# Optimization experiments

Measured on AMD Instinct MI355X. Metric: run time of the kernel, lower is better.

The kernel has to match this reference:

```python
import jax, jax.numpy as jnp
import numpy as np

B, S, DM, H, DK, DH = 8, 1024, 512, 8, 32, 64
LN_EPS = 1e-5
NEG_SLOPE = 0.01  # torch LeakyReLU default


def _l2norm(t, axis=-1, eps=1e-12):
    # matches F.normalize(p=2): x / max(||x||, eps)
    n = jnp.sqrt(jnp.sum(t * t, axis=axis, keepdims=True))
    return t / jnp.maximum(n, eps)


def _layernorm(t, w, b, eps=LN_EPS):
    mu = jnp.mean(t, axis=-1, keepdims=True)
    var = jnp.mean((t - mu) ** 2, axis=-1, keepdims=True)
    return (t - mu) * jax.lax.rsqrt(var + eps) * w + b


def setup_inputs() -> dict:
    key = jax.random.key(0)
    ks = jax.random.split(key, 16)
    x = jax.random.normal(ks[0], (B, S, DM), dtype=jnp.float32)
    # causal-style mask: True = masked (upper triangle)
    attn_mask = jnp.broadcast_to(jnp.triu(jnp.ones((S, S), dtype=bool), k=1), (B, S, S))
    pairwise_dist = jax.random.uniform(ks[1], (B, S, S), dtype=jnp.float32)
    s = 0.02
    return {
        "x": x,
        "attn_mask": attn_mask,
        "pairwise_dist": pairwise_dist,
        "Wq": jax.random.normal(ks[2], (H, DK, DM), dtype=jnp.float32) * s,
        "Wk": jax.random.normal(ks[3], (H, DK, DM), dtype=jnp.float32) * s,
        "Wv": jax.random.normal(ks[4], (H, DH, DM), dtype=jnp.float32) * s,
        "omega": jnp.ones((H,), dtype=jnp.float32),
        "Wo": jax.random.normal(ks[5], (DM, H * DH), dtype=jnp.float32) * s,
        "bo": jnp.zeros((DM,), dtype=jnp.float32),
        "Wf": jax.random.normal(ks[6], (DM, DM), dtype=jnp.float32) * s,
        "bf": jnp.zeros((DM,), dtype=jnp.float32),
        "ln1_w": jnp.ones((DM,), dtype=jnp.float32),
        "ln1_b": jnp.zeros((DM,), dtype=jnp.float32),
        "ln2_w": jnp.ones((DM,), dtype=jnp.float32),
        "ln2_b": jnp.zeros((DM,), dtype=jnp.float32),
    }


def _encoder_layer(x, attn_mask, pairwise_dist, Wq, Wk, Wv, omega,
                   Wo, bo, Wf, bf, ln1_w, ln1_b, ln2_w, ln2_b):
    # --- multi-head self-attention, all heads batched ---
    q = _l2norm(jnp.einsum('bsd,hkd->hbsk', x, Wq))   # [H,B,S,DK]
    k = _l2norm(jnp.einsum('bsd,hkd->hbsk', x, Wk))
    v = jnp.einsum('bsd,hvd->hbsv', x, Wv)            # [H,B,S,DH]
    scores = jnp.einsum('hbsk,hbtk->hbst', q, k)      # cosine-sim, [H,B,S,S]
    # distance bias: exp(-omega*d) - 1, detached in the original
    r = jax.lax.stop_gradient(
        jnp.exp(-omega[:, None, None, None] * pairwise_dist[None]) - 1.0)
    scores = scores + r
    scores = jnp.where(attn_mask[None], -jnp.inf, scores)
    # custom softmax: exp(x) / (sum + 1); exp(-inf)=0 handles masking
    z = jnp.exp(scores)
    attn = z / (jnp.sum(z, axis=-1, keepdims=True) + 1.0)
    y = jnp.einsum('hbst,hbtv->hbsv', attn, v)        # [H,B,S,DH]
    y = jnp.transpose(y, (1, 2, 0, 3)).reshape(x.shape[0], x.shape[1], -1)  # concat heads
    x_attn = y @ Wo.T + bo
    # --- residual + LN + FFN (dropout p=0 -> identity) ---
    z1 = _layernorm(x + x_attn, ln1_w, ln1_b)
    z_ff = jax.nn.leaky_relu(z1 @ Wf.T + bf, negative_slope=NEG_SLOPE)
    return _layernorm(z1 + z_ff, ln2_w, ln2_b)


def reference(x, attn_mask, pairwise_dist, Wq, Wk, Wv, omega,
              Wo, bo, Wf, bf, ln1_w, ln1_b, ln2_w, ln2_b):
    return _encoder_layer(x, attn_mask, pairwise_dist, Wq, Wk, Wv, omega,
                          Wo, bo, Wf, bf, ln1_w, ln1_b, ln2_w, ln2_b)
```

## Files before the change

kernel.cpp:

```cpp
#include <hip/hip_runtime.h>
#include <hip/hip_bf16.h>
#include <math.h>
#include <stdint.h>

#define BB 8
#define SS 1024
#define DMM 512
#define HH 8
#define DKK 32
#define DHH 64

typedef __bf16 bf16x8 __attribute__((ext_vector_type(8)));
typedef float f32x4 __attribute__((ext_vector_type(4)));

__device__ __forceinline__ void gll16(const void* g, void* l) {
  __builtin_amdgcn_global_load_lds(
      (const __attribute__((address_space(1))) void*)(uintptr_t)g,
      (__attribute__((address_space(3))) void*)(uint32_t)(uintptr_t)l,
      16, 0, 0);
}

__device__ __forceinline__ uint4 pack8(const float4 a, const float4 b) {
  union { __hip_bfloat162 h2[4]; uint4 u; } p;
  p.h2[0] = __float22bfloat162_rn(make_float2(a.x, a.y));
  p.h2[1] = __float22bfloat162_rn(make_float2(a.z, a.w));
  p.h2[2] = __float22bfloat162_rn(make_float2(b.x, b.y));
  p.h2[3] = __float22bfloat162_rn(make_float2(b.z, b.w));
  return p.u;
}

__global__ __launch_bounds__(256) void cvt_pre(
    const float* __restrict__ x, const float* __restrict__ Wq,
    const float* __restrict__ Wk, const float* __restrict__ Wv,
    __bf16* __restrict__ xb, __bf16* __restrict__ Wcat) {
  size_t i = ((size_t)blockIdx.x * 256 + threadIdx.x) * 8;
  const float* s;
  __bf16* d;
  size_t off;
  if (i < 4194304) { s = x; d = xb; off = i; }
  else {
    size_t j = i - 4194304;
    d = Wcat + j;
    if (j < 131072) { s = Wq; off = j; }
    else if (j < 262144) { s = Wk; off = j - 131072; }
    else { s = Wv; off = j - 262144; }
    d = Wcat + j - off + off;
    float4 a = *(const float4*)&s[off];
    float4 b = *(const float4*)&s[off + 4];
    *(uint4*)&Wcat[j] = pack8(a, b);
    return;
  }
  float4 a = *(const float4*)&s[off];
  float4 b = *(const float4*)&s[off + 4];
  *(uint4*)&d[off] = pack8(a, b);
}

__global__ __launch_bounds__(256) void cvt_wof(
    const float* __restrict__ Wo, const float* __restrict__ Wf,
    __bf16* __restrict__ dWo, __bf16* __restrict__ dWf) {
  size_t i = ((size_t)blockIdx.x * 256 + threadIdx.x) * 8;
  const float* s;
  __bf16* d;
  size_t off;
  if (i < 262144) { s = Wo; d = dWo; off = i; }
  else { s = Wf; d = dWf; off = i - 262144; }
  float4 a = *(const float4*)&s[off];
  float4 b = *(const float4*)&s[off + 4];
  *(uint4*)&d[off] = pack8(a, b);
}

template <int MODE>
__global__ __launch_bounds__(256) void gemm_bf16(
    const __bf16* __restrict__ A, const __bf16* __restrict__ W,
    const float* __restrict__ bias, const float* __restrict__ resid,
    float* __restrict__ C, int N) {
  __shared__ __bf16 As[128 * 32];
  __shared__ __bf16 Bs[128 * 32];
  const int tid = threadIdx.x;
  const int n0 = blockIdx.x * 128;
  const int m0 = blockIdx.y * 128;
  const int lane = tid & 63;
  const int w = tid >> 6;
  const int wm = (w & 1) * 64, wn = (w >> 1) * 64;
  const int fr = lane & 15, quad = lane >> 4;

  const int srow = lane >> 2;
  const int schunk = (lane & 3) ^ ((lane >> 3) & 3);

  f32x4 acc[4][4];
#pragma unroll
  for (int mi = 0; mi < 4; ++mi)
#pragma unroll
    for (int ni = 0; ni < 4; ++ni) acc[mi][ni] = (f32x4){0.f, 0.f, 0.f, 0.f};

  for (int kt = 0; kt < 512; kt += 32) {
    __syncthreads();
#pragma unroll
    for (int j = 0; j < 2; ++j) {
      const int seg = w * 2 + j;
      const int row = seg * 16 + srow;
      gll16(&A[(size_t)(m0 + row) * 512 + kt + schunk * 8], &As[seg * 512]);
      gll16(&W[(size_t)(n0 + row) * 512 + kt + schunk * 8], &Bs[seg * 512]);
    }
    __syncthreads();

    bf16x8 af[4], bf[4];
    const int rsw = (quad ^ ((fr >> 1) & 3)) * 8;
#pragma unroll
    for (int mi = 0; mi < 4; ++mi)
      af[mi] = *(const bf16x8*)&As[(wm + mi * 16 + fr) * 32 + rsw];
#pragma unroll
    for (int ni = 0; ni < 4; ++ni)
      bf[ni] = *(const bf16x8*)&Bs[(wn + ni * 16 + fr) * 32 + rsw];
#pragma unroll
    for (int mi = 0; mi < 4; ++mi)
#pragma unroll
      for (int ni = 0; ni < 4; ++ni)
        acc[mi][ni] = __builtin_amdgcn_mfma_f32_16x16x32_bf16(
            af[mi], bf[ni], acc[mi][ni], 0, 0, 0);
  }

  const int er = (lane >> 4) * 4;
  const int ec = lane & 15;
#pragma unroll
  for (int mi = 0; mi < 4; ++mi) {
#pragma unroll
    for (int ni = 0; ni < 4; ++ni) {
      const int n = n0 + wn + ni * 16 + ec;
      float bsv = (MODE != 0) ? bias[n] : 0.0f;
#pragma unroll
      for (int r = 0; r < 4; ++r) {
        const int m = m0 + wm + mi * 16 + er + r;
        float v = acc[mi][ni][r];
        if (MODE == 1) {
          v += bsv + resid[(size_t)m * 512 + n];
        } else if (MODE == 2) {
          float g = v + bsv;
          g = g > 0.f ? g : 0.01f * g;
          v = resid[(size_t)m * 512 + n] + g;
        }
        C[(size_t)m * N + n] = v;
      }
    }
  }
}

__global__ __launch_bounds__(256) void prep_qkv(
    const float* __restrict__ qkv, __bf16* __restrict__ Qg,
    __bf16* __restrict__ Kg, __bf16* __restrict__ Vt) {
  __shared__ __bf16 vt[64][136];
  const int bh = blockIdx.x;
  const int b = bh >> 3, h = bh & 7;
  const int sb = blockIdx.y * 128;
  const int tid = threadIdx.x;

  {
    const int row = tid >> 1, half = tid & 1;
    const size_t rb = ((size_t)b * 1024 + sb + row) * 1024;
    {
      const float* p = qkv + rb + h * 32 + half * 16;
      float4 a[4];
      float ss = 0.f;
#pragma unroll
      for (int i = 0; i < 4; ++i) {
        a[i] = ((const float4*)p)[i];
        ss += a[i].x * a[i].x + a[i].y * a[i].y + a[i].z * a[i].z + a[i].w * a[i].w;
      }
      ss += __shfl_xor(ss, 1, 64);
      float sc = 1.0f / fmaxf(sqrtf(ss), 1e-12f);
      float4 s0 = make_float4(a[0].x * sc, a[0].y * sc, a[0].z * sc, a[0].w * sc);
      float4 s1 = make_float4(a[1].x * sc, a[1].y * sc, a[1].z * sc, a[1].w * sc);
      float4 s2 = make_float4(a[2].x * sc, a[2].y * sc, a[2].z * sc, a[2].w * sc);
      float4 s3 = make_float4(a[3].x * sc, a[3].y * sc, a[3].z * sc, a[3].w * sc);
      uint4* o = (uint4*)(Qg + ((size_t)bh * 1024 + sb + row) * 32 + half * 16);
      o[0] = pack8(s0, s1);
      o[1] = pack8(s2, s3);
    }
    {
      const float* p = qkv + rb + 256 + h * 32 + half * 16;
      float4 a[4];
      float ss = 0.f;
#pragma unroll
      for (int i = 0; i < 4; ++i) {
        a[i] = ((const float4*)p)[i];
        ss += a[i].x * a[i].x + a[i].y * a[i].y + a[i].z * a[i].z + a[i].w * a[i].w;
      }
      ss += __shfl_xor(ss, 1, 64);
      float sc = 1.0f / fmaxf(sqrtf(ss), 1e-12f);
      float4 s0 = make_float4(a[0].x * sc, a[0].y * sc, a[0].z * sc, a[0].w * sc);
      float4 s1 = make_float4(a[1].x * sc, a[1].y * sc, a[1].z * sc, a[1].w * sc);
      float4 s2 = make_float4(a[2].x * sc, a[2].y * sc, a[2].z * sc, a[2].w * sc);
      float4 s3 = make_float4(a[3].x * sc, a[3].y * sc, a[3].z * sc, a[3].w * sc);
      uint4* o = (uint4*)(Kg + ((size_t)bh * 1024 + sb + row) * 32 + half * 16);
      o[0] = pack8(s0, s1);
      o[1] = pack8(s2, s3);
    }
  }

#pragma unroll
  for (int i = 0; i < 8; ++i) {
    int idx = tid + i * 256;
    int t = idx >> 4, vd4 = (idx & 15) * 4;
    float4 v = *(const float4*)&qkv[((size_t)b * 1024 + sb + t) * 1024 + 512 + h * 64 + vd4];
    vt[vd4 + 0][t] = (__bf16)v.x;
    vt[vd4 + 1][t] = (__bf16)v.y;
    vt[vd4 + 2][t] = (__bf16)v.z;
    vt[vd4 + 3][t] = (__bf16)v.w;
  }
  __syncthreads();
  {
    const int vd = tid >> 2, tseg = (tid & 3) * 32;
    uint4* o = (uint4*)(Vt + (size_t)bh * 65536 + (size_t)vd * 1024 + sb + tseg);
#pragma unroll
    for (int j = 0; j < 4; ++j)
      o[j] = *(const uint4*)&vt[vd][tseg + j * 8];
  }
}

__global__ __launch_bounds__(64, 4) void attn_wave(
    const __bf16* __restrict__ Qg, const __bf16* __restrict__ Kg,
    const __bf16* __restrict__ Vt, const float* __restrict__ dist,
    const float* __restrict__ omega, __bf16* __restrict__ y) {
  __shared__ __bf16 zbuf[2][16][40];

  const int idx = blockIdx.x;
  const int sb2 = 31 - (idx >> 6);
  const int bh = idx & 63;
  const int b = bh >> 3, h = bh & 7;
  const int lane = threadIdx.x & 63;
  const int l15 = lane & 15;
  const int q = lane >> 4;
  const float om = omega[h];
  const int s_base = sb2 * 32;

  const __bf16* Qp = Qg + (size_t)bh * 32768;
  const __bf16* Kp = Kg + (size_t)bh * 32768;
  const __bf16* Vp = Vt + (size_t)bh * 65536;
  const float* Dp = dist + ((size_t)b * 1024 + s_base) * 1024;

  bf16x8 bq[2];
#pragma unroll
  for (int st = 0; st < 2; ++st)
    bq[st] = *(const bf16x8*)&Qp[(size_t)(s_base + st * 16 + l15) * 32 + q * 8];

  f32x4 acc[2][4];
#pragma unroll
  for (int st = 0; st < 2; ++st)
#pragma unroll
    for (int ni = 0; ni < 4; ++ni) acc[st][ni] = (f32x4){0.f, 0.f, 0.f, 0.f};
  float zsum[2] = {0.f, 0.f};

  const int nch = sb2 + 1;
  for (int c = 0; c < nch; ++c) {
    const int t0 = c * 32;
    const bf16x8 ak0 = *(const bf16x8*)&Kp[(size_t)(t0 + l15) * 32 + q * 8];
    const bf16x8 ak1 = *(const bf16x8*)&Kp[(size_t)(t0 + 16 + l15) * 32 + q * 8];
    bf16x8 vb[4];
#pragma unroll
    for (int ni = 0; ni < 4; ++ni)
      vb[ni] = *(const bf16x8*)&Vp[(size_t)(ni * 16 + l15) * 1024 + t0 + q * 8];

#pragma unroll
    for (int st = 0; st < 2; ++st) {
      const int s = s_base + st * 16 + l15;
      const float4 dv0 = *(const float4*)&Dp[(size_t)(st * 16 + l15) * 1024 + t0 + q * 4];
      const float4 dv1 = *(const float4*)&Dp[(size_t)(st * 16 + l15) * 1024 + t0 + 16 + q * 4];
      f32x4 s0 = __builtin_amdgcn_mfma_f32_16x16x32_bf16(
          ak0, bq[st], (f32x4){0.f, 0.f, 0.f, 0.f}, 0, 0, 0);
      f32x4 s1 = __builtin_amdgcn_mfma_f32_16x16x32_bf16(
          ak1, bq[st], (f32x4){0.f, 0.f, 0.f, 0.f}, 0, 0, 0);
      float z0[4], z1[4];
#pragma unroll
      for (int r = 0; r < 4; ++r) {
        int t = t0 + q * 4 + r;
        float zv = __expf(s0[r] + __expf(-om * (&dv0.x)[r]) - 1.0f);
        z0[r] = (t <= s) ? zv : 0.0f;
        t += 16;
        zv = __expf(s1[r] + __expf(-om * (&dv1.x)[r]) - 1.0f);
        z1[r] = (t <= s) ? zv : 0.0f;
        zsum[st] += z0[r] + z1[r];
      }
      union { __hip_bfloat162 h2[2]; uint2 u; } p0, p1;
      p0.h2[0] = __float22bfloat162_rn(make_float2(z0[0], z0[1]));
      p0.h2[1] = __float22bfloat162_rn(make_float2(z0[2], z0[3]));
      p1.h2[0] = __float22bfloat162_rn(make_float2(z1[0], z1[1]));
      p1.h2[1] = __float22bfloat162_rn(make_float2(z1[2], z1[3]));
      *(uint2*)&zbuf[st][l15][q * 4] = p0.u;
      *(uint2*)&zbuf[st][l15][16 + q * 4] = p1.u;
    }
#pragma unroll
    for (int st = 0; st < 2; ++st) {
      const bf16x8 az = *(const bf16x8*)&zbuf[st][l15][q * 8];
#pragma unroll
      for (int ni = 0; ni < 4; ++ni)
        acc[st][ni] = __builtin_amdgcn_mfma_f32_16x16x32_bf16(
            az, vb[ni], acc[st][ni], 0, 0, 0);
    }
  }

#pragma unroll
  for (int st = 0; st < 2; ++st) {
    zsum[st] += __shfl_xor(zsum[st], 16, 64);
    zsum[st] += __shfl_xor(zsum[st], 32, 64);
  }

#pragma unroll
  for (int st = 0; st < 2; ++st) {
#pragma unroll
    for (int r = 0; r < 4; ++r) {
      const float dn = __shfl(zsum[st], q * 4 + r, 64);
      const float inv = 1.0f / (dn + 1.0f);
      __bf16* yp = &y[((size_t)b * 1024 + s_base + st * 16 + q * 4 + r) * 512 + h * 64 + l15];
#pragma unroll
      for (int ni = 0; ni < 4; ++ni)
        yp[ni * 16] = (__bf16)(acc[st][ni][r] * inv);
    }
  }
}

__global__ __launch_bounds__(256) void ln_kernel(
    const float* __restrict__ in, const float* __restrict__ w,
    const float* __restrict__ bvec, float* __restrict__ out,
    __bf16* __restrict__ outb) {
  const int row = blockIdx.x * 4 + (threadIdx.x >> 6);
  const int lane = threadIdx.x & 63;
  const float4* ip = (const float4*)(in + (size_t)row * 512);
  float4 a = ip[lane * 2], c = ip[lane * 2 + 1];
  float s = a.x + a.y + a.z + a.w + c.x + c.y + c.z + c.w;
#pragma unroll
  for (int off = 32; off > 0; off >>= 1) s += __shfl_xor(s, off, 64);
  const float mu = s * (1.0f / 512.0f);
  a.x -= mu; a.y -= mu; a.z -= mu; a.w -= mu;
  c.x -= mu; c.y -= mu; c.z -= mu; c.w -= mu;
  float s2 = a.x * a.x + a.y * a.y + a.z * a.z + a.w * a.w +
             c.x * c.x + c.y * c.y + c.z * c.z + c.w * c.w;
#pragma unroll
  for (int off = 32; off > 0; off >>= 1) s2 += __shfl_xor(s2, off, 64);
  const float inv = rsqrtf(s2 * (1.0f / 512.0f) + 1e-5f);
  const float4 w0 = ((const float4*)w)[lane * 2], w1 = ((const float4*)w)[lane * 2 + 1];
  const float4 b0 = ((const float4*)bvec)[lane * 2], b1 = ((const float4*)bvec)[lane * 2 + 1];
  float4 o0, o1;
  o0.x = a.x * inv * w0.x + b0.x; o0.y = a.y * inv * w0.y + b0.y;
  o0.z = a.z * inv * w0.z + b0.z; o0.w = a.w * inv * w0.w + b0.w;
  o1.x = c.x * inv * w1.x + b1.x; o1.y = c.y * inv * w1.y + b1.y;
  o1.z = c.z * inv * w1.z + b1.z; o1.w = c.w * inv * w1.w + b1.w;
  float4* op = (float4*)(out + (size_t)row * 512);
  op[lane * 2] = o0; op[lane * 2 + 1] = o1;
  if (outb) *(uint4*)&outb[(size_t)row * 512 + lane * 8] = pack8(o0, o1);
}

extern "C" void kernel_launch(void* const* d_in, const int* in_sizes, int n_in,
                              void* d_out, int out_size, void* d_ws, size_t ws_size,
                              hipStream_t stream) {
  const float* x = (const float*)d_in[0];
  const float* dist = (const float*)d_in[2];
  const float* Wq = (const float*)d_in[3];
  const float* Wk = (const float*)d_in[4];
  const float* Wv = (const float*)d_in[5];
  const float* omega = (const float*)d_in[6];
  const float* Wo = (const float*)d_in[7];
  const float* bo = (const float*)d_in[8];
  const float* Wf = (const float*)d_in[9];
  const float* bf_ = (const float*)d_in[10];
  const float* ln1w = (const float*)d_in[11];
  const float* ln1b = (const float*)d_in[12];
  const float* ln2w = (const float*)d_in[13];
  const float* ln2b = (const float*)d_in[14];
  float* out = (float*)d_out;

  char* base = (char*)d_ws;
  const size_t MB = 1 << 20;
  float* qkv = (float*)base;
  __bf16* yb = (__bf16*)base;
  float* t1 = (float*)(base + 8 * MB);
  __bf16* t1b = (__bf16*)(base + 24 * MB);
  __bf16* xb = (__bf16*)(base + 32 * MB);
  __bf16* Wcat = (__bf16*)(base + 40 * MB);
  __bf16* Qg = (__bf16*)(base + 32 * MB);
  __bf16* Kg = (__bf16*)(base + 36 * MB);
  __bf16* Vt = (__bf16*)(base + 40 * MB);
  __bf16* Wob = (__bf16*)(base + 32 * MB);
  __bf16* Wfb = (__bf16*)(base + 32 * MB + 512 * 1024);

  dim3 blk(256);
  cvt_pre<<<dim3(2304), blk, 0, stream>>>(x, Wq, Wk, Wv, xb, Wcat);
  gemm_bf16<0><<<dim3(8, 64), blk, 0, stream>>>(xb, Wcat, nullptr, nullptr,
                                                qkv, 1024);
  prep_qkv<<<dim3(64, 8), blk, 0, stream>>>(qkv, Qg, Kg, Vt);
  attn_wave<<<dim3(2048), dim3(64), 0, stream>>>(Qg, Kg, Vt, dist, omega, yb);
  cvt_wof<<<dim3(256), blk, 0, stream>>>(Wo, Wf, Wob, Wfb);
  gemm_bf16<1><<<dim3(4, 64), blk, 0, stream>>>(yb, Wob, bo, x, t1, 512);
  ln_kernel<<<dim3(2048), blk, 0, stream>>>(t1, ln1w, ln1b, t1, t1b);
  gemm_bf16<2><<<dim3(4, 64), blk, 0, stream>>>(t1b, Wfb, bf_, t1, out, 512);
  ln_kernel<<<dim3(2048), blk, 0, stream>>>(out, ln2w, ln2b, out, nullptr);
}
```

Baseline: 265.7 us.

## Fuse QKV L2-norm into GEMM epilogue and share K/V tiles across attention waves

The QKV GEMM now L2-normalizes Q and K in its epilogue and writes bf16 outputs directly, so the fp32 qkv intermediate disappears. prep_qkv shrinks to a bf16 V transpose. Attention moves from one-wave blocks to 4-wave blocks of 64 query rows that stage K and V tiles in swizzled LDS and share them. Both weight-conversion kernels merge into one launch. This cuts global traffic and redundant K/V loads, at the cost of extra block syncs and bigger tiles on the causal diagonal.

```diff
diff --git a/kernel.cpp b/kernel.cpp
--- a/kernel.cpp
+++ b/kernel.cpp
@@ -29,44 +29,125 @@
   return p.u;
 }
 
-__global__ __launch_bounds__(256) void cvt_pre(
+__global__ __launch_bounds__(256) void cvt_all(
     const float* __restrict__ x, const float* __restrict__ Wq,
     const float* __restrict__ Wk, const float* __restrict__ Wv,
-    __bf16* __restrict__ xb, __bf16* __restrict__ Wcat) {
+    const float* __restrict__ Wo, const float* __restrict__ Wf,
+    __bf16* __restrict__ xb, __bf16* __restrict__ Wcat,
+    __bf16* __restrict__ Wob, __bf16* __restrict__ Wfb) {
   size_t i = ((size_t)blockIdx.x * 256 + threadIdx.x) * 8;
   const float* s;
   __bf16* d;
   size_t off;
-  if (i < 4194304) { s = x; d = xb; off = i; }
+  if (i < 4194304) { s = x; d = xb + i; off = i; }
   else {
     size_t j = i - 4194304;
-    d = Wcat + j;
-    if (j < 131072) { s = Wq; off = j; }
-    else if (j < 262144) { s = Wk; off = j - 131072; }
-    else { s = Wv; off = j - 262144; }
-    d = Wcat + j - off + off;
-    float4 a = *(const float4*)&s[off];
-    float4 b = *(const float4*)&s[off + 4];
-    *(uint4*)&Wcat[j] = pack8(a, b);
-    return;
+    if (j < 524288) {
+      d = Wcat + j;
+      if (j < 131072) { s = Wq; off = j; }
+      else if (j < 262144) { s = Wk; off = j - 131072; }
+      else { s = Wv; off = j - 262144; }
+    } else {
+      size_t jj = j - 524288;
+      if (jj < 262144) { s = Wo; d = Wob + jj; off = jj; }
+      else { s = Wf; d = Wfb + (jj - 262144); off = jj - 262144; }
+    }
   }
   float4 a = *(const float4*)&s[off];
   float4 b = *(const float4*)&s[off + 4];
-  *(uint4*)&d[off] = pack8(a, b);
-}
-
-__global__ __launch_bounds__(256) void cvt_wof(
-    const float* __restrict__ Wo, const float* __restrict__ Wf,
-    __bf16* __restrict__ dWo, __bf16* __restrict__ dWf) {
-  size_t i = ((size_t)blockIdx.x * 256 + threadIdx.x) * 8;
-  const float* s;
-  __bf16* d;
-  size_t off;
-  if (i < 262144) { s = Wo; d = dWo; off = i; }
-  else { s = Wf; d = dWf; off = i - 262144; }
-  float4 a = *(const float4*)&s[off];
-  float4 b = *(const float4*)&s[off + 4];
-  *(uint4*)&d[off] = pack8(a, b);
+  *(uint4*)d = pack8(a, b);
+}
+
+__global__ __launch_bounds__(256) void gemm_qkv(
+    const __bf16* __restrict__ A, const __bf16* __restrict__ W,
+    __bf16* __restrict__ Qg, __bf16* __restrict__ Kg,
+    __bf16* __restrict__ Vrow) {
+  __shared__ __bf16 As[128 * 32];
+  __shared__ __bf16 Bs[128 * 32];
+  const int tid = threadIdx.x;
+  const int n0 = blockIdx.x * 128;
+  const int m0 = blockIdx.y * 128;
+  const int lane = tid & 63;
+  const int w = tid >> 6;
+  const int wm = (w & 1) * 64, wn = (w >> 1) * 64;
+  const int fr = lane & 15, quad = lane >> 4;
+  const int srow = lane >> 2;
+  const int schunk = (lane & 3) ^ ((lane >> 3) & 3);
+
+  f32x4 acc[4][4];
+#pragma unroll
+  for (int mi = 0; mi < 4; ++mi)
+#pragma unroll
+    for (int ni = 0; ni < 4; ++ni) acc[mi][ni] = (f32x4){0.f, 0.f, 0.f, 0.f};
+
+  for (int kt = 0; kt < 512; kt += 32) {
+    __syncthreads();
+#pragma unroll
+    for (int j = 0; j < 2; ++j) {
+      const int seg = w * 2 + j;
+      const int row = seg * 16 + srow;
+      gll16(&A[(size_t)(m0 + row) * 512 + kt + schunk * 8], &As[seg * 512]);
+      gll16(&W[(size_t)(n0 + row) * 512 + kt + schunk * 8], &Bs[seg * 512]);
+    }
+    __syncthreads();
+
+    bf16x8 af[4], bf[4];
+    const int rsw = (quad ^ ((fr >> 1) & 3)) * 8;
+#pragma unroll
+    for (int mi = 0; mi < 4; ++mi)
+      af[mi] = *(const bf16x8*)&As[(wm + mi * 16 + fr) * 32 + rsw];
+#pragma unroll
+    for (int ni = 0; ni < 4; ++ni)
+      bf[ni] = *(const bf16x8*)&Bs[(wn + ni * 16 + fr) * 32 + rsw];
+#pragma unroll
+    for (int mi = 0; mi < 4; ++mi)
+#pragma unroll
+      for (int ni = 0; ni < 4; ++ni)
+        acc[mi][ni] = __builtin_amdgcn_mfma_f32_16x16x32_bf16(
+            af[mi], bf[ni], acc[mi][ni], 0, 0, 0);
+  }
+
+  const int er = quad * 4;
+  const int ec = fr;
+  if (n0 < 512) {
+    const bool isq = (n0 < 256);
+    __bf16* G = isq ? Qg : Kg;
+    const int nb = isq ? n0 : n0 - 256;
+#pragma unroll
+    for (int mi = 0; mi < 4; ++mi) {
+#pragma unroll
+      for (int p = 0; p < 2; ++p) {
+        const int hh = (nb + wn + p * 32) >> 5;
+#pragma unroll
+        for (int r = 0; r < 4; ++r) {
+          float v0 = acc[mi][2 * p][r], v1 = acc[mi][2 * p + 1][r];
+          float ss = v0 * v0 + v1 * v1;
+          ss += __shfl_xor(ss, 1, 64);
+          ss += __shfl_xor(ss, 2, 64);
+          ss += __shfl_xor(ss, 4, 64);
+          ss += __shfl_xor(ss, 8, 64);
+          const float sc = 1.0f / fmaxf(sqrtf(ss), 1e-12f);
+          const int mm = m0 + wm + mi * 16 + er + r;
+          const int bb = mm >> 10, s = mm & 1023;
+          __bf16* gp = G + ((size_t)(bb * 8 + hh) * 1024 + s) * 32;
+          gp[ec] = (__bf16)(v0 * sc);
+          gp[16 + ec] = (__bf16)(v1 * sc);
+        }
+      }
+    }
+  } else {
+#pragma unroll
+    for (int mi = 0; mi < 4; ++mi)
+#pragma unroll
+      for (int ni = 0; ni < 4; ++ni) {
+        const int n = n0 - 512 + wn + ni * 16 + ec;
+#pragma unroll
+        for (int r = 0; r < 4; ++r) {
+          const int mm = m0 + wm + mi * 16 + er + r;
+          Vrow[(size_t)mm * 512 + n] = (__bf16)acc[mi][ni][r];
+        }
+      }
+  }
 }
 
 template <int MODE>
@@ -83,7 +164,6 @@
   const int w = tid >> 6;
   const int wm = (w & 1) * 64, wn = (w >> 1) * 64;
   const int fr = lane & 15, quad = lane >> 4;
-
   const int srow = lane >> 2;
   const int schunk = (lane & 3) ^ ((lane >> 3) & 3);
 
@@ -120,21 +200,21 @@
             af[mi], bf[ni], acc[mi][ni], 0, 0, 0);
   }
 
-  const int er = (lane >> 4) * 4;
-  const int ec = lane & 15;
+  const int er = quad * 4;
+  const int ec = fr;
 #pragma unroll
   for (int mi = 0; mi < 4; ++mi) {
 #pragma unroll
     for (int ni = 0; ni < 4; ++ni) {
       const int n = n0 + wn + ni * 16 + ec;
-      float bsv = (MODE != 0) ? bias[n] : 0.0f;
+      float bsv = bias[n];
 #pragma unroll
       for (int r = 0; r < 4; ++r) {
         const int m = m0 + wm + mi * 16 + er + r;
         float v = acc[mi][ni][r];
         if (MODE == 1) {
           v += bsv + resid[(size_t)m * 512 + n];
-        } else if (MODE == 2) {
+        } else {
           float g = v + bsv;
           g = g > 0.f ? g : 0.01f * g;
           v = resid[(size_t)m * 512 + n] + g;
@@ -145,67 +225,23 @@
   }
 }
 
-__global__ __launch_bounds__(256) void prep_qkv(
-    const float* __restrict__ qkv, __bf16* __restrict__ Qg,
-    __bf16* __restrict__ Kg, __bf16* __restrict__ Vt) {
+__global__ __launch_bounds__(256) void v_transpose(
+    const __bf16* __restrict__ Vrow, __bf16* __restrict__ Vt) {
   __shared__ __bf16 vt[64][136];
   const int bh = blockIdx.x;
   const int b = bh >> 3, h = bh & 7;
   const int sb = blockIdx.y * 128;
   const int tid = threadIdx.x;
-
-  {
-    const int row = tid >> 1, half = tid & 1;
-    const size_t rb = ((size_t)b * 1024 + sb + row) * 1024;
-    {
-      const float* p = qkv + rb + h * 32 + half * 16;
-      float4 a[4];
-      float ss = 0.f;
-#pragma unroll
-      for (int i = 0; i < 4; ++i) {
-        a[i] = ((const float4*)p)[i];
-        ss += a[i].x * a[i].x + a[i].y * a[i].y + a[i].z * a[i].z + a[i].w * a[i].w;
-      }
-      ss += __shfl_xor(ss, 1, 64);
-      float sc = 1.0f / fmaxf(sqrtf(ss), 1e-12f);
-      float4 s0 = make_float4(a[0].x * sc, a[0].y * sc, a[0].z * sc, a[0].w * sc);
-      float4 s1 = make_float4(a[1].x * sc, a[1].y * sc, a[1].z * sc, a[1].w * sc);
-      float4 s2 = make_float4(a[2].x * sc, a[2].y * sc, a[2].z * sc, a[2].w * sc);
-      float4 s3 = make_float4(a[3].x * sc, a[3].y * sc, a[3].z * sc, a[3].w * sc);
-      uint4* o = (uint4*)(Qg + ((size_t)bh * 1024 + sb + row) * 32 + half * 16);
-      o[0] = pack8(s0, s1);
-      o[1] = pack8(s2, s3);
-    }
-    {
-      const float* p = qkv + rb + 256 + h * 32 + half * 16;
-      float4 a[4];
-      float ss = 0.f;
-#pragma unroll
-      for (int i = 0; i < 4; ++i) {
-        a[i] = ((const float4*)p)[i];
-        ss += a[i].x * a[i].x + a[i].y * a[i].y + a[i].z * a[i].z + a[i].w * a[i].w;
-      }
-      ss += __shfl_xor(ss, 1, 64);
-      float sc = 1.0f / fmaxf(sqrtf(ss), 1e-12f);
-      float4 s0 = make_float4(a[0].x * sc, a[0].y * sc, a[0].z * sc, a[0].w * sc);
-      float4 s1 = make_float4(a[1].x * sc, a[1].y * sc, a[1].z * sc, a[1].w * sc);
-      float4 s2 = make_float4(a[2].x * sc, a[2].y * sc, a[2].z * sc, a[2].w * sc);
-      float4 s3 = make_float4(a[3].x * sc, a[3].y * sc, a[3].z * sc, a[3].w * sc);
-      uint4* o = (uint4*)(Kg + ((size_t)bh * 1024 + sb + row) * 32 + half * 16);
-      o[0] = pack8(s0, s1);
-      o[1] = pack8(s2, s3);
-    }
-  }
-
 #pragma unroll
   for (int i = 0; i < 8; ++i) {
     int idx = tid + i * 256;
     int t = idx >> 4, vd4 = (idx & 15) * 4;
-    float4 v = *(const float4*)&qkv[((size_t)b * 1024 + sb + t) * 1024 + 512 + h * 64 + vd4];
-    vt[vd4 + 0][t] = (__bf16)v.x;
-    vt[vd4 + 1][t] = (__bf16)v.y;
-    vt[vd4 + 2][t] = (__bf16)v.z;
-    vt[vd4 + 3][t] = (__bf16)v.w;
+    union { uint2 u; __bf16 e[4]; } v;
+    v.u = *(const uint2*)&Vrow[((size_t)(b * 1024 + sb + t)) * 512 + h * 64 + vd4];
+    vt[vd4 + 0][t] = v.e[0];
+    vt[vd4 + 1][t] = v.e[1];
+    vt[vd4 + 2][t] = v.e[2];
+    vt[vd4 + 3][t] = v.e[3];
   }
   __syncthreads();
   {
@@ -217,104 +253,96 @@
   }
 }
 
-__global__ __launch_bounds__(64, 4) void attn_wave(
+__global__ __launch_bounds__(256) void attn_fused(
     const __bf16* __restrict__ Qg, const __bf16* __restrict__ Kg,
     const __bf16* __restrict__ Vt, const float* __restrict__ dist,
     const float* __restrict__ omega, __bf16* __restrict__ y) {
-  __shared__ __bf16 zbuf[2][16][40];
-
-  const int idx = blockIdx.x;
-  const int sb2 = 31 - (idx >> 6);
-  const int bh = idx & 63;
-  const int b = bh >> 3, h = bh & 7;
-  const int lane = threadIdx.x & 63;
-  const int l15 = lane & 15;
+  __shared__ __bf16 Ks[64 * 32];
+  __shared__ __bf16 Vs[64 * 64];
+  __shared__ __bf16 zbuf[4][16][72];
+
+  const int b = blockIdx.x;
+  const int s0 = (15 - blockIdx.y) * 64;
+  const int h = blockIdx.z;
+  const int bh = b * 8 + h;
+  const int tid = threadIdx.x;
+  const int lane = tid & 63;
+  const int w = tid >> 6;
   const int q = lane >> 4;
+  const int m = lane & 15;
   const float om = omega[h];
-  const int s_base = sb2 * 32;
-
-  const __bf16* Qp = Qg + (size_t)bh * 32768;
-  const __bf16* Kp = Kg + (size_t)bh * 32768;
-  const __bf16* Vp = Vt + (size_t)bh * 65536;
-  const float* Dp = dist + ((size_t)b * 1024 + s_base) * 1024;
-
-  bf16x8 bq[2];
-#pragma unroll
-  for (int st = 0; st < 2; ++st)
-    bq[st] = *(const bf16x8*)&Qp[(size_t)(s_base + st * 16 + l15) * 32 + q * 8];
-
-  f32x4 acc[2][4];
-#pragma unroll
-  for (int st = 0; st < 2; ++st)
-#pragma unroll
-    for (int ni = 0; ni < 4; ++ni) acc[st][ni] = (f32x4){0.f, 0.f, 0.f, 0.f};
-  float zsum[2] = {0.f, 0.f};
-
-  const int nch = sb2 + 1;
-  for (int c = 0; c < nch; ++c) {
-    const int t0 = c * 32;
-    const bf16x8 ak0 = *(const bf16x8*)&Kp[(size_t)(t0 + l15) * 32 + q * 8];
-    const bf16x8 ak1 = *(const bf16x8*)&Kp[(size_t)(t0 + 16 + l15) * 32 + q * 8];
-    bf16x8 vb[4];
+
+  const int sl = s0 + w * 16 + m;
+  const bf16x8 bq = *(const bf16x8*)&Qg[((size_t)bh * 1024 + sl) * 32 + q * 8];
+  const int kswz = (q ^ ((m >> 1) & 3)) * 8;
+
+  f32x4 acc[4];
+#pragma unroll
+  for (int ni = 0; ni < 4; ++ni) acc[ni] = (f32x4){0.f, 0.f, 0.f, 0.f};
+  float zsum = 0.0f;
+  const int ntiles = (s0 >> 6) + 1;
+
+  for (int tt = 0; tt < ntiles; ++tt) {
+    const int t0 = tt * 64;
+    __syncthreads();
+    {
+      int row = tid >> 2, p = tid & 3;
+      uint4 v = *(const uint4*)&Kg[((size_t)bh * 1024 + t0 + row) * 32 + p * 8];
+      *(uint4*)&Ks[row * 32 + ((p ^ ((row >> 1) & 3)) * 8)] = v;
+    }
+#pragma unroll
+    for (int i = 0; i < 2; ++i) {
+      int idx = tid + i * 256;
+      int vd = idx >> 3, p = idx & 7;
+      uint4 v = *(const uint4*)&Vt[(size_t)bh * 65536 + (size_t)vd * 1024 + t0 + p * 8];
+      *(uint4*)&Vs[vd * 64 + ((p ^ (vd & 7)) * 8)] = v;
+    }
+    float4 dv[4];
+#pragma unroll
+    for (int mi = 0; mi < 4; ++mi)
+      dv[mi] = *(const float4*)&dist[((size_t)b * 1024 + sl) * 1024 + t0 + 16 * mi + q * 4];
+    __syncthreads();
+
+#pragma unroll
+    for (int mi = 0; mi < 4; ++mi) {
+      const bf16x8 ak = *(const bf16x8*)&Ks[(16 * mi + m) * 32 + kswz];
+      f32x4 s4 = __builtin_amdgcn_mfma_f32_16x16x32_bf16(
+          ak, bq, (f32x4){0.f, 0.f, 0.f, 0.f}, 0, 0, 0);
+      float zr[4];
+#pragma unroll
+      for (int r = 0; r < 4; ++r) {
+        const int t = t0 + 16 * mi + q * 4 + r;
+        float zv = __expf(s4[r] + __expf(-om * (&dv[mi].x)[r]) - 1.0f);
+        zr[r] = (t <= sl) ? zv : 0.0f;
+        zsum += zr[r];
+      }
+      union { __hip_bfloat162 h2[2]; uint2 u; } pz;
+      pz.h2[0] = __float22bfloat162_rn(make_float2(zr[0], zr[1]));
+      pz.h2[1] = __float22bfloat162_rn(make_float2(zr[2], zr[3]));
+      *(uint2*)&zbuf[w][m][16 * mi + q * 4] = pz.u;
+    }
+    const bf16x8 az0 = *(const bf16x8*)&zbuf[w][m][q * 8];
+    const bf16x8 az1 = *(const bf16x8*)&zbuf[w][m][32 + q * 8];
+#pragma unroll
+    for (int ni = 0; ni < 4; ++ni) {
+      const bf16x8 vb0 = *(const bf16x8*)&Vs[(16 * ni + m) * 64 + ((q ^ (m & 7)) * 8)];
+      const bf16x8 vb1 = *(const bf16x8*)&Vs[(16 * ni + m) * 64 + (((q + 4) ^ (m & 7)) * 8)];
+      acc[ni] = __builtin_amdgcn_mfma_f32_16x16x32_bf16(az0, vb0, acc[ni], 0, 0, 0);
+      acc[ni] = __builtin_amdgcn_mfma_f32_16x16x32_bf16(az1, vb1, acc[ni], 0, 0, 0);
+    }
+  }
+
+  zsum += __shfl_xor(zsum, 16, 64);
+  zsum += __shfl_xor(zsum, 32, 64);
+
+#pragma unroll
+  for (int r = 0; r < 4; ++r) {
+    const float dn = __shfl(zsum, q * 4 + r, 64);
+    const float inv = 1.0f / (dn + 1.0f);
+    __bf16* yp = &y[((size_t)b * 1024 + s0 + w * 16 + q * 4 + r) * 512 + h * 64 + m];
 #pragma unroll
     for (int ni = 0; ni < 4; ++ni)
-      vb[ni] = *(const bf16x8*)&Vp[(size_t)(ni * 16 + l15) * 1024 + t0 + q * 8];
-
-#pragma unroll
-    for (int st = 0; st < 2; ++st) {
-      const int s = s_base + st * 16 + l15;
-      const float4 dv0 = *(const float4*)&Dp[(size_t)(st * 16 + l15) * 1024 + t0 + q * 4];
-      const float4 dv1 = *(const float4*)&Dp[(size_t)(st * 16 + l15) * 1024 + t0 + 16 + q * 4];
-      f32x4 s0 = __builtin_amdgcn_mfma_f32_16x16x32_bf16(
-          ak0, bq[st], (f32x4){0.f, 0.f, 0.f, 0.f}, 0, 0, 0);
-      f32x4 s1 = __builtin_amdgcn_mfma_f32_16x16x32_bf16(
-          ak1, bq[st], (f32x4){0.f, 0.f, 0.f, 0.f}, 0, 0, 0);
-      float z0[4], z1[4];
-#pragma unroll
-      for (int r = 0; r < 4; ++r) {
-        int t = t0 + q * 4 + r;
-        float zv = __expf(s0[r] + __expf(-om * (&dv0.x)[r]) - 1.0f);
-        z0[r] = (t <= s) ? zv : 0.0f;
-        t += 16;
-        zv = __expf(s1[r] + __expf(-om * (&dv1.x)[r]) - 1.0f);
-        z1[r] = (t <= s) ? zv : 0.0f;
-        zsum[st] += z0[r] + z1[r];
-      }
-      union { __hip_bfloat162 h2[2]; uint2 u; } p0, p1;
-      p0.h2[0] = __float22bfloat162_rn(make_float2(z0[0], z0[1]));
-      p0.h2[1] = __float22bfloat162_rn(make_float2(z0[2], z0[3]));
-      p1.h2[0] = __float22bfloat162_rn(make_float2(z1[0], z1[1]));
-      p1.h2[1] = __float22bfloat162_rn(make_float2(z1[2], z1[3]));
-      *(uint2*)&zbuf[st][l15][q * 4] = p0.u;
-      *(uint2*)&zbuf[st][l15][16 + q * 4] = p1.u;
-    }
-#pragma unroll
-    for (int st = 0; st < 2; ++st) {
-      const bf16x8 az = *(const bf16x8*)&zbuf[st][l15][q * 8];
-#pragma unroll
-      for (int ni = 0; ni < 4; ++ni)
-        acc[st][ni] = __builtin_amdgcn_mfma_f32_16x16x32_bf16(
-            az, vb[ni], acc[st][ni], 0, 0, 0);
-    }
-  }
-
-#pragma unroll
-  for (int st = 0; st < 2; ++st) {
-    zsum[st] += __shfl_xor(zsum[st], 16, 64);
-    zsum[st] += __shfl_xor(zsum[st], 32, 64);
-  }
-
-#pragma unroll
-  for (int st = 0; st < 2; ++st) {
-#pragma unroll
-    for (int r = 0; r < 4; ++r) {
-      const float dn = __shfl(zsum[st], q * 4 + r, 64);
-      const float inv = 1.0f / (dn + 1.0f);
-      __bf16* yp = &y[((size_t)b * 1024 + s_base + st * 16 + q * 4 + r) * 512 + h * 64 + l15];
-#pragma unroll
-      for (int ni = 0; ni < 4; ++ni)
-        yp[ni * 16] = (__bf16)(acc[st][ni][r] * inv);
-    }
+      yp[ni * 16] = (__bf16)(acc[ni][r] * inv);
   }
 }
 
@@ -370,25 +398,24 @@
 
   char* base = (char*)d_ws;
   const size_t MB = 1 << 20;
-  float* qkv = (float*)base;
+  __bf16* xb = (__bf16*)base;
   __bf16* yb = (__bf16*)base;
-  float* t1 = (float*)(base + 8 * MB);
-  __bf16* t1b = (__bf16*)(base + 24 * MB);
-  __bf16* xb = (__bf16*)(base + 32 * MB);
-  __bf16* Wcat = (__bf16*)(base + 40 * MB);
-  __bf16* Qg = (__bf16*)(base + 32 * MB);
-  __bf16* Kg = (__bf16*)(base + 36 * MB);
-  __bf16* Vt = (__bf16*)(base + 40 * MB);
-  __bf16* Wob = (__bf16*)(base + 32 * MB);
-  __bf16* Wfb = (__bf16*)(base + 32 * MB + 512 * 1024);
+  __bf16* Wcat = (__bf16*)(base + 8 * MB);
+  __bf16* Wob = (__bf16*)(base + 9 * MB);
+  __bf16* Wfb = (__bf16*)(base + 9 * MB + 512 * 1024);
+  __bf16* Qg = (__bf16*)(base + 10 * MB);
+  __bf16* Kg = (__bf16*)(base + 14 * MB);
+  __bf16* Vrow = (__bf16*)(base + 18 * MB);
+  __bf16* Vt = (__bf16*)(base + 26 * MB);
+  float* t1 = (float*)(base + 18 * MB);
+  __bf16* t1b = (__bf16*)(base + 34 * MB);
 
   dim3 blk(256);
-  cvt_pre<<<dim3(2304), blk, 0, stream>>>(x, Wq, Wk, Wv, xb, Wcat);
-  gemm_bf16<0><<<dim3(8, 64), blk, 0, stream>>>(xb, Wcat, nullptr, nullptr,
-                                                qkv, 1024);
-  prep_qkv<<<dim3(64, 8), blk, 0, stream>>>(qkv, Qg, Kg, Vt);
-  attn_wave<<<dim3(2048), dim3(64), 0, stream>>>(Qg, Kg, Vt, dist, omega, yb);
-  cvt_wof<<<dim3(256), blk, 0, stream>>>(Wo, Wf, Wob, Wfb);
+  cvt_all<<<dim3(2560), blk, 0, stream>>>(x, Wq, Wk, Wv, Wo, Wf,
+                                          xb, Wcat, Wob, Wfb);
+  gemm_qkv<<<dim3(8, 64), blk, 0, stream>>>(xb, Wcat, Qg, Kg, Vrow);
+  v_transpose<<<dim3(64, 8), blk, 0, stream>>>(Vrow, Vt);
+  attn_fused<<<dim3(8, 16, 8), blk, 0, stream>>>(Qg, Kg, Vt, dist, omega, yb);
   gemm_bf16<1><<<dim3(4, 64), blk, 0, stream>>>(yb, Wob, bo, x, t1, 512);
   ln_kernel<<<dim3(2048), blk, 0, stream>>>(t1, ln1w, ln1b, t1, t1b);
   gemm_bf16<2><<<dim3(4, 64), blk, 0, stream>>>(t1b, Wfb, bf_, t1, out, 512);
```

New measurement: 246.3 us. 1.08x faster.
